# Kernel optimization log

Measured on AMD Instinct MI355X. Metric: run time of the kernel, lower is better.

## Reference

```python
import jax, jax.numpy as jnp
import numpy as np

EMBED_DIM = 256
NUM_CODES = 8192
COMMIT_COST = 0.25


def setup_inputs() -> dict:
    key = jax.random.key(0)
    k1, k2 = jax.random.split(key)
    x = jax.random.normal(k1, (16, 1024, EMBED_DIM), dtype=jnp.float32)
    # torch init is uniform(-1/K, 1/K); use small-scale normal-like init via uniform
    codebook = jax.random.uniform(k2, (NUM_CODES, EMBED_DIM), dtype=jnp.float32,
                                  minval=-1.0 / NUM_CODES, maxval=1.0 / NUM_CODES)
    return {"x": x, "codebook": codebook}


def reference(x, codebook):
    # x: [B, S, D], codebook: [K, D]
    input_shape = x.shape
    flat = x.reshape(-1, EMBED_DIM)  # [N, D]
    distances = (jnp.sum(flat * flat, axis=1, keepdims=True)
                 + jnp.sum(codebook * codebook, axis=1)
                 - 2.0 * jnp.matmul(flat, codebook.T))
    encoding_indices = jnp.argmin(distances, axis=1)  # [N]
    # one-hot @ codebook is just a gather
    quantized = jnp.take(codebook, encoding_indices, axis=0).reshape(input_shape)
    # training w/ EMA: commitment loss only (codebook updated via EMA buffers, not grad)
    commitment_loss = COMMIT_COST * jnp.mean(
        (jax.lax.stop_gradient(quantized) - x) ** 2)
    # straight-through estimator
    quantized_st = x + jax.lax.stop_gradient(quantized - x)
    indices = encoding_indices.reshape(input_shape[:-1])
    return quantized_st, indices, commitment_loss
```

## Files before the change

kernel.cpp:

```cpp
#include <hip/hip_runtime.h>

#define D 256
#define KCODES 8192
#define NTOK 16384
#define QSIZE (NTOK * D)
#define NBLK 128
#define CBS 64
#define TH 2e-4f
#define CBSCALE 4096.0f
#define UNSCALE2 4.8828125e-4f
#define CCAP 4096

typedef _Float16 f16x8 __attribute__((ext_vector_type(8)));
typedef float f32x4 __attribute__((ext_vector_type(4)));
typedef __attribute__((address_space(3))) void* lds_vp;
typedef __attribute__((address_space(1))) const void* gbl_vp;

#define P2_LDS (256 * 65 * 4)

__device__ __forceinline__ ushort f32_to_bf16(float f) {
    unsigned u = __float_as_uint(f);
    return (ushort)((u + 0x7FFFu + ((u >> 16) & 1)) >> 16);
}
__device__ __forceinline__ float bf16_to_f32(ushort h) {
    return __uint_as_float((unsigned)h << 16);
}
__device__ __forceinline__ ushort f32_to_f16(float f) {
    _Float16 h = (_Float16)f;
    ushort u; __builtin_memcpy(&u, &h, 2);
    return u;
}
__device__ __forceinline__ float rdlane(float v, int lane) {
    return __uint_as_float(__builtin_amdgcn_readlane(__float_as_uint(v), lane));
}

__global__ __launch_bounds__(256) void cvtx_kernel(const float* __restrict__ x,
                                                   ushort* __restrict__ xb,
                                                   float* __restrict__ xsq) {
    int i = blockIdx.x * 256 + threadIdx.x;
    float4 v = reinterpret_cast<const float4*>(x)[i];
    ushort4 o;
    o.x = f32_to_f16(v.x); o.y = f32_to_f16(v.y);
    o.z = f32_to_f16(v.z); o.w = f32_to_f16(v.w);
    reinterpret_cast<ushort4*>(xb)[i] = o;
    float s = v.x * v.x + v.y * v.y + v.z * v.z + v.w * v.w;
#pragma unroll
    for (int off = 32; off > 0; off >>= 1) s += __shfl_down(s, off);
    if ((threadIdx.x & 63) == 0) xsq[i >> 6] = s;
}

__global__ __launch_bounds__(256) void e2_kernel(const float* __restrict__ cb,
                                                 float* __restrict__ e2) {
    int c = blockIdx.x * 4 + (threadIdx.x >> 6);
    int lane = threadIdx.x & 63;
    float4 v = reinterpret_cast<const float4*>(cb + (size_t)c * D)[lane];
    float s = v.x * v.x + v.y * v.y + v.z * v.z + v.w * v.w;
#pragma unroll
    for (int off = 32; off > 0; off >>= 1) s += __shfl_down(s, off);
    if (lane == 0) e2[c] = s;
}

__global__ __launch_bounds__(256, 3) void pass1_kernel(
    const ushort* __restrict__ xb, const float* __restrict__ cb,
    const float* __restrict__ e2, unsigned* __restrict__ screen) {
    __shared__ ushort ash[2][128 * 32];
    __shared__ ushort bsh[2][128 * 32];
    const int tid = threadIdx.x;
    const int w = tid >> 6, l = tid & 63;
    const int wr = w >> 1, wc = w & 1;
    const int t0 = blockIdx.x * 128, n0 = blockIdx.y * 128;

    f32x4 acc[4][4];
#pragma unroll
    for (int mt = 0; mt < 4; ++mt)
#pragma unroll
        for (int nt = 0; nt < 4; ++nt) acc[mt][nt] = (f32x4)0.f;

    const int byte0 = w * 2048 + l * 16;
    const int row0 = byte0 >> 6, c80 = (byte0 >> 4) & 3;
    const int byte1 = byte0 + 1024;
    const int row1 = byte1 >> 6, c81 = (byte1 >> 4) & 3;
    const ushort* ga0 = xb + (size_t)(t0 + row0) * D + c80 * 8;
    const ushort* ga1 = xb + (size_t)(t0 + row1) * D + c81 * 8;
    const int brow = tid >> 1, bkh = (tid & 1) * 16;
    const float* gB = cb + (size_t)(n0 + brow) * D + bkh;
    float4 rb[4];

#define STAGE_A(KT, BUF)                                                                   \
    do {                                                                                   \
        __builtin_amdgcn_global_load_lds((gbl_vp)(ga0 + (KT) * 32),                        \
                                         (lds_vp)(&ash[BUF][w * 1024]), 16, 0, 0);         \
        __builtin_amdgcn_global_load_lds((gbl_vp)(ga1 + (KT) * 32),                        \
                                         (lds_vp)(&ash[BUF][w * 1024 + 512]), 16, 0, 0);   \
    } while (0)
#define LOAD_B(KT)                                                                         \
    do {                                                                                   \
        const float4* p = reinterpret_cast<const float4*>(gB + (KT) * 32);                 \
        rb[0] = p[0]; rb[1] = p[1]; rb[2] = p[2]; rb[3] = p[3];                            \
    } while (0)
#define WRITE_B(BUF)                                                                       \
    do {                                                                                   \
        unsigned q[8];                                                                     \
        _Pragma("unroll")                                                                  \
        for (int e = 0; e < 4; ++e) {                                                      \
            q[2 * e] = (unsigned)f32_to_f16(rb[e].x * CBSCALE) |                           \
                       ((unsigned)f32_to_f16(rb[e].y * CBSCALE) << 16);                    \
            q[2 * e + 1] = (unsigned)f32_to_f16(rb[e].z * CBSCALE) |                       \
                           ((unsigned)f32_to_f16(rb[e].w * CBSCALE) << 16);                \
        }                                                                                  \
        uint4* dst = reinterpret_cast<uint4*>(&bsh[BUF][brow * 32 + bkh]);                 \
        uint4 q0; q0.x = q[0]; q0.y = q[1]; q0.z = q[2]; q0.w = q[3];                      \
        uint4 q1; q1.x = q[4]; q1.y = q[5]; q1.z = q[6]; q1.w = q[7];                      \
        dst[0] = q0; dst[1] = q1;                                                          \
    } while (0)

    LOAD_B(0);
    STAGE_A(0, 0);
    WRITE_B(0);
    __syncthreads();
#pragma unroll
    for (int kt = 0; kt < 8; ++kt) {
        const int cur = kt & 1;
        if (kt < 7) { LOAD_B(kt + 1); STAGE_A(kt + 1, cur ^ 1); }
        const ushort* xbase = &ash[cur][0] + (wr * 64 + (l & 15)) * 32 + (l >> 4) * 8;
        const ushort* cbase = &bsh[cur][0] + (wc * 64 + (l & 15)) * 32 + (l >> 4) * 8;
        f16x8 a[4], b[4];
#pragma unroll
        for (int mt = 0; mt < 4; ++mt)
            a[mt] = *reinterpret_cast<const f16x8*>(xbase + mt * 16 * 32);
#pragma unroll
        for (int nt = 0; nt < 4; ++nt)
            b[nt] = *reinterpret_cast<const f16x8*>(cbase + nt * 16 * 32);
#pragma unroll
        for (int mt = 0; mt < 4; ++mt)
#pragma unroll
            for (int nt = 0; nt < 4; ++nt)
                acc[mt][nt] = __builtin_amdgcn_mfma_f32_16x16x32_f16(
                    a[mt], b[nt], acc[mt][nt], 0, 0, 0);
        if (kt < 7) WRITE_B(cur ^ 1);
        __syncthreads();
    }
#undef STAGE_A
#undef LOAD_B
#undef WRITE_B

    float e2v[4];
#pragma unroll
    for (int nt = 0; nt < 4; ++nt)
        e2v[nt] = e2[n0 + wc * 64 + nt * 16 + (l & 15)];
    const int nb64 = blockIdx.y * 2 + wc;
#pragma unroll
    for (int mt = 0; mt < 4; ++mt) {
#pragma unroll
        for (int r = 0; r < 4; ++r) {
            float v1 = fmaf(-UNSCALE2, acc[mt][0][r], e2v[0]);
            float v2 = 3.4e38f;
            int a1 = (l & 15);
#pragma unroll
            for (int nt = 1; nt < 4; ++nt) {
                float f = fmaf(-UNSCALE2, acc[mt][nt][r], e2v[nt]);
                int idx = nt * 16 + (l & 15);
                bool lt = f < v1;
                v2 = lt ? v1 : fminf(v2, f);
                a1 = lt ? idx : a1;
                v1 = lt ? f : v1;
            }
#pragma unroll
            for (int off = 1; off < 16; off <<= 1) {
                float ov1 = __shfl_xor(v1, off);
                float ov2 = __shfl_xor(v2, off);
                int oa1 = __shfl_xor(a1, off);
                float nv2 = fminf(fminf(v2, ov2), fmaxf(v1, ov1));
                bool take = ov1 < v1;
                v1 = take ? ov1 : v1;
                a1 = take ? oa1 : a1;
                v2 = nv2;
            }
            if ((l & 15) == 0) {
                int token = t0 + wr * 64 + mt * 16 + (l >> 4) * 4 + r;
                ushort m1b = f32_to_bf16(v1);
                unsigned big = (v2 - bf16_to_f32(m1b) > TH) ? 1u : 0u;
                screen[(size_t)token * NBLK + nb64] =
                    ((unsigned)m1b << 16) | ((unsigned)a1 << 1) | big;
            }
        }
    }
}

__global__ __launch_bounds__(256) void pass2a_kernel(
    const unsigned* __restrict__ screen, unsigned long long* __restrict__ bestKey,
    unsigned* __restrict__ cand, unsigned* __restrict__ counts,
    float* __restrict__ out) {
    const int tid = threadIdx.x;
    const int w = tid >> 6, l = tid & 63;
    const int token = blockIdx.x * 4 + w;
    if (blockIdx.x == 0 && tid == 0) out[(size_t)QSIZE + NTOK] = 0.f;

    uint2 u2 = reinterpret_cast<const uint2*>(screen + (size_t)token * NBLK)[l];
    float ma = bf16_to_f32((ushort)(u2.x >> 16));
    float mb = bf16_to_f32((ushort)(u2.y >> 16));
    float v1, v2; unsigned pk; int blk;
    if (mb < ma) { v1 = mb; v2 = ma; pk = u2.y; blk = 2 * l + 1; }
    else         { v1 = ma; v2 = mb; pk = u2.x; blk = 2 * l; }
#pragma unroll
    for (int off = 1; off < 64; off <<= 1) {
        float ov1 = __shfl_xor(v1, off);
        float ov2 = __shfl_xor(v2, off);
        unsigned opk = __shfl_xor(pk, off);
        int oblk = __shfl_xor(blk, off);
        float nv2 = fminf(fminf(v2, ov2), fmaxf(v1, ov1));
        bool take = ov1 < v1;
        v1 = take ? ov1 : v1;
        pk = take ? opk : pk;
        blk = take ? oblk : blk;
        v2 = nv2;
    }
    bool decided = ((pk & 1u) != 0u) && (v2 - v1 > TH);
    if (l == 0)
        bestKey[token] = decided
            ? (unsigned long long)(unsigned)(blk * 64 + (int)((pk >> 1) & 63u))
            : 0xFFFFFFFFFFFFFFFFULL;
    if (!decided) {
        float thr = v1 + TH;
        if (ma <= thr) {
            unsigned s = atomicAdd(&counts[2 * l], 1u);
            if (s < CCAP) cand[(size_t)(2 * l) * CCAP + s] = (unsigned)token;
        }
        if (mb <= thr) {
            unsigned s = atomicAdd(&counts[2 * l + 1], 1u);
            if (s < CCAP) cand[(size_t)(2 * l + 1) * CCAP + s] = (unsigned)token;
        }
    }
}

__global__ __launch_bounds__(256, 2) void pass2b_kernel(
    const float* __restrict__ x, const float* __restrict__ cb,
    const float* __restrict__ e2, const float* __restrict__ xsq,
    const unsigned* __restrict__ cand, const unsigned* __restrict__ counts,
    unsigned long long* __restrict__ bestKey) {
    extern __shared__ float csh[];
    const int tid = threadIdx.x;
    const int nb = blockIdx.x >> 2;
    const int quarter = blockIdx.x & 3;
    int cnt = (int)counts[nb];
    if (cnt > CCAP) cnt = CCAP;
    if (quarter * 16 >= cnt) return;

#pragma unroll
    for (int r = 0; r < 16; ++r) {
        int i = r * 256 + tid;
        int row = i >> 6, kq = i & 63;
        float4 v = reinterpret_cast<const float4*>(cb + (size_t)(nb * CBS + row) * D)[kq];
        csh[(kq * 4 + 0) * 65 + row] = v.x;
        csh[(kq * 4 + 1) * 65 + row] = v.y;
        csh[(kq * 4 + 2) * 65 + row] = v.z;
        csh[(kq * 4 + 3) * 65 + row] = v.w;
    }
    __syncthreads();

    const int w = tid >> 6, j = tid & 63;
    const float e2v = e2[nb * CBS + j];
    const int ci0 = nb * CBS + j;
    const float4* X4 = reinterpret_cast<const float4*>(x);
    const unsigned* clist = cand + (size_t)nb * CCAP;
    const int slot = quarter * 4 + w;
    const int p0 = slot * 4;
    if (p0 >= cnt) return;

    for (int p = p0; p < cnt; p += 64) {
        int i1 = p + 1 < cnt ? p + 1 : cnt - 1;
        int i2 = p + 2 < cnt ? p + 2 : cnt - 1;
        int i3 = p + 3 < cnt ? p + 3 : cnt - 1;
        int t0 = (int)clist[p],  t1 = (int)clist[i1];
        int t2 = (int)clist[i2], t3 = (int)clist[i3];
        float4 v0 = X4[(size_t)t0 * 64 + j];
        float4 v1 = X4[(size_t)t1 * 64 + j];
        float4 v2 = X4[(size_t)t2 * 64 + j];
        float4 v3 = X4[(size_t)t3 * 64 + j];
        float a0 = 0.f, a1 = 0.f, a2 = 0.f, a3 = 0.f;
#pragma unroll
        for (int kq = 0; kq < 64; ++kq) {
            float c0 = csh[(kq * 4 + 0) * 65 + j];
            float c1 = csh[(kq * 4 + 1) * 65 + j];
            float c2 = csh[(kq * 4 + 2) * 65 + j];
            float c3 = csh[(kq * 4 + 3) * 65 + j];
            a0 = fmaf(rdlane(v0.x, kq), c0, a0);
            a0 = fmaf(rdlane(v0.y, kq), c1, a0);
            a0 = fmaf(rdlane(v0.z, kq), c2, a0);
            a0 = fmaf(rdlane(v0.w, kq), c3, a0);
            a1 = fmaf(rdlane(v1.x, kq), c0, a1);
            a1 = fmaf(rdlane(v1.y, kq), c1, a1);
            a1 = fmaf(rdlane(v1.z, kq), c2, a1);
            a1 = fmaf(rdlane(v1.w, kq), c3, a1);
            a2 = fmaf(rdlane(v2.x, kq), c0, a2);
            a2 = fmaf(rdlane(v2.y, kq), c1, a2);
            a2 = fmaf(rdlane(v2.z, kq), c2, a2);
            a2 = fmaf(rdlane(v2.w, kq), c3, a2);
            a3 = fmaf(rdlane(v3.x, kq), c0, a3);
            a3 = fmaf(rdlane(v3.y, kq), c1, a3);
            a3 = fmaf(rdlane(v3.z, kq), c2, a3);
            a3 = fmaf(rdlane(v3.w, kq), c3, a3);
        }
        float av[4] = {a0, a1, a2, a3};
        int tv[4] = {t0, t1, t2, t3};
#pragma unroll
        for (int g = 0; g < 4; ++g) {
            float dd = fmaf(-2.f, av[g], xsq[tv[g]] + e2v);
            int ci = ci0;
#pragma unroll
            for (int off = 1; off < 64; off <<= 1) {
                float od = __shfl_xor(dd, off);
                int oc = __shfl_xor(ci, off);
                if (od < dd || (od == dd && oc < ci)) { dd = od; ci = oc; }
            }
            if (j == 0) {
                unsigned u = __float_as_uint(dd);
                u = (u & 0x80000000u) ? ~u : (u | 0x80000000u);
                unsigned long long key =
                    ((unsigned long long)u << 32) | (unsigned)ci;
                atomicMin(bestKey + tv[g], key);
            }
        }
    }
}

__global__ __launch_bounds__(256) void gather_kernel(
    const float* __restrict__ x, const float* __restrict__ cb,
    const unsigned long long* __restrict__ bestKey,
    float* __restrict__ out, float* __restrict__ partial) {
    __shared__ float red[4];
    const int token = blockIdx.x;
    const int tid = threadIdx.x;
    int idx = (int)(bestKey[token] & 0xFFFFFFFFULL);
    if ((unsigned)idx >= (unsigned)KCODES) idx = 0;
    float q = cb[(size_t)idx * D + tid];
    float xv = x[(size_t)token * D + tid];
    out[(size_t)token * D + tid] = q;
    float d = q - xv;
    d = d * d;
#pragma unroll
    for (int off = 32; off > 0; off >>= 1) d += __shfl_down(d, off);
    if ((tid & 63) == 0) red[tid >> 6] = d;
    __syncthreads();
    if (tid == 0) {
        partial[token] = red[0] + red[1] + red[2] + red[3];
        out[(size_t)QSIZE + token] = (float)idx;
    }
}

__global__ __launch_bounds__(256) void loss_kernel(const float* __restrict__ partial,
                                                   float* __restrict__ out) {
    __shared__ float red[4];
    int gid = blockIdx.x * 256 + threadIdx.x;
    float s = partial[gid];
#pragma unroll
    for (int off = 32; off > 0; off >>= 1) s += __shfl_down(s, off);
    if ((threadIdx.x & 63) == 0) red[threadIdx.x >> 6] = s;
    __syncthreads();
    if (threadIdx.x == 0) {
        float total = red[0] + red[1] + red[2] + red[3];
        atomicAdd(out + (size_t)QSIZE + NTOK, 0.25f * total / (float)QSIZE);
    }
}

extern "C" void kernel_launch(void* const* d_in, const int* in_sizes, int n_in,
                              void* d_out, int out_size, void* d_ws, size_t ws_size,
                              hipStream_t stream) {
    const float* x = (const float*)d_in[0];
    const float* cb = (const float*)d_in[1];
    float* out = (float*)d_out;
    float* ws = (float*)d_ws;

    ushort* xb = (ushort*)d_out;
    unsigned* screen = (unsigned*)((char*)d_out + 8388608);
    unsigned* cand = (unsigned*)d_out;

    float* e2 = ws;
    float* xsq = ws + 8192;
    unsigned* counts = (unsigned*)(ws + 8192 + 16384);
    float* partial = ws + 8192 + 2 * 16384;
    unsigned long long* bestKey = (unsigned long long*)(ws + 8192 + 3 * 16384);

    hipFuncSetAttribute((const void*)pass2b_kernel,
                        hipFuncAttributeMaxDynamicSharedMemorySize, P2_LDS);

    cvtx_kernel<<<QSIZE / 1024, 256, 0, stream>>>(x, xb, xsq);
    e2_kernel<<<KCODES / 4, 256, 0, stream>>>(cb, e2);
    pass1_kernel<<<dim3(NTOK / 128, KCODES / 128), 256, 0, stream>>>(xb, cb, e2, screen);
    hipMemsetAsync(counts, 0, NBLK * sizeof(unsigned), stream);
    pass2a_kernel<<<NTOK / 4, 256, 0, stream>>>(screen, bestKey, cand, counts, out);
    pass2b_kernel<<<4 * NBLK, 256, P2_LDS, stream>>>(
        x, cb, e2, xsq, cand, counts, bestKey);
    gather_kernel<<<NTOK, 256, 0, stream>>>(x, cb, bestKey, out, partial);
    loss_kernel<<<NTOK / 256, 256, 0, stream>>>(partial, out);
}
```

Measured before the change: 354.1 us.

## Keep codebook tile resident in LDS and loop over token tiles in pass1

Pass1 now converts a full 128x256 codebook tile to fp16 once per block and keeps it in LDS with an XOR swizzle. Each block then streams 16 token tiles through a double-buffered A stage. Previously every 128x128 output tile reloaded and reconverted its fp32 codebook slice. The aim is to cut repeated global codebook reads and conversion work. In exchange the grid shrinks to 8x64 blocks, occupancy drops to 2 blocks per CU, and the prologue is serialized.

```diff
diff --git a/kernel.cpp b/kernel.cpp
--- a/kernel.cpp
+++ b/kernel.cpp
@@ -16,6 +16,7 @@
 typedef __attribute__((address_space(3))) void* lds_vp;
 typedef __attribute__((address_space(1))) const void* gbl_vp;
 
+#define P1_LDS (128 * 256 * 2 + 2 * 128 * 32 * 2)
 #define P2_LDS (256 * 65 * 4)
 
 __device__ __forceinline__ ushort f32_to_bf16(float f) {
@@ -60,131 +61,135 @@
     if (lane == 0) e2[c] = s;
 }
 
-__global__ __launch_bounds__(256, 3) void pass1_kernel(
+__global__ __launch_bounds__(256, 2) void pass1_kernel(
     const ushort* __restrict__ xb, const float* __restrict__ cb,
     const float* __restrict__ e2, unsigned* __restrict__ screen) {
-    __shared__ ushort ash[2][128 * 32];
-    __shared__ ushort bsh[2][128 * 32];
+    extern __shared__ ushort sm[];
+    ushort* Bsh = sm;
+    ushort* Ash = sm + 128 * 256;
     const int tid = threadIdx.x;
     const int w = tid >> 6, l = tid & 63;
     const int wr = w >> 1, wc = w & 1;
-    const int t0 = blockIdx.x * 128, n0 = blockIdx.y * 128;
-
-    f32x4 acc[4][4];
-#pragma unroll
-    for (int mt = 0; mt < 4; ++mt)
-#pragma unroll
-        for (int nt = 0; nt < 4; ++nt) acc[mt][nt] = (f32x4)0.f;
-
-    const int byte0 = w * 2048 + l * 16;
-    const int row0 = byte0 >> 6, c80 = (byte0 >> 4) & 3;
-    const int byte1 = byte0 + 1024;
-    const int row1 = byte1 >> 6, c81 = (byte1 >> 4) & 3;
-    const ushort* ga0 = xb + (size_t)(t0 + row0) * D + c80 * 8;
-    const ushort* ga1 = xb + (size_t)(t0 + row1) * D + c81 * 8;
-    const int brow = tid >> 1, bkh = (tid & 1) * 16;
-    const float* gB = cb + (size_t)(n0 + brow) * D + bkh;
-    float4 rb[4];
-
-#define STAGE_A(KT, BUF)                                                                   \
+    const int n0 = blockIdx.y * 128;
+    const int tc0 = blockIdx.x * (NTOK / 8);
+
+#pragma unroll
+    for (int j = 0; j < 16; ++j) {
+        int c = tid + j * 256;
+        int row = c >> 5, slot = c & 31;
+        const float4* grow = reinterpret_cast<const float4*>(cb + (size_t)(n0 + row) * D);
+        float4 f0 = grow[slot * 2];
+        float4 f1 = grow[slot * 2 + 1];
+        uint4 q;
+        q.x = (unsigned)f32_to_f16(f0.x * CBSCALE) |
+              ((unsigned)f32_to_f16(f0.y * CBSCALE) << 16);
+        q.y = (unsigned)f32_to_f16(f0.z * CBSCALE) |
+              ((unsigned)f32_to_f16(f0.w * CBSCALE) << 16);
+        q.z = (unsigned)f32_to_f16(f1.x * CBSCALE) |
+              ((unsigned)f32_to_f16(f1.y * CBSCALE) << 16);
+        q.w = (unsigned)f32_to_f16(f1.z * CBSCALE) |
+              ((unsigned)f32_to_f16(f1.w * CBSCALE) << 16);
+        int sw = slot ^ (row & 7);
+        *reinterpret_cast<uint4*>(Bsh + row * 256 + sw * 8) = q;
+    }
+
+    const int arow0 = w * 32 + (l >> 2);
+    const int arow1 = arow0 + 16;
+    const int asg8 = (((l & 3) ^ ((l >> 3) & 3)) << 3);
+
+#define STAGE_A(TB, KT, BUF)                                                               \
     do {                                                                                   \
-        __builtin_amdgcn_global_load_lds((gbl_vp)(ga0 + (KT) * 32),                        \
-                                         (lds_vp)(&ash[BUF][w * 1024]), 16, 0, 0);         \
-        __builtin_amdgcn_global_load_lds((gbl_vp)(ga1 + (KT) * 32),                        \
-                                         (lds_vp)(&ash[BUF][w * 1024 + 512]), 16, 0, 0);   \
+        __builtin_amdgcn_global_load_lds(                                                  \
+            (gbl_vp)(xb + (size_t)((TB) + arow0) * D + (KT) * 32 + asg8),                  \
+            (lds_vp)(Ash + (BUF) * 4096 + w * 1024), 16, 0, 0);                            \
+        __builtin_amdgcn_global_load_lds(                                                  \
+            (gbl_vp)(xb + (size_t)((TB) + arow1) * D + (KT) * 32 + asg8),                  \
+            (lds_vp)(Ash + (BUF) * 4096 + w * 1024 + 512), 16, 0, 0);                      \
     } while (0)
-#define LOAD_B(KT)                                                                         \
-    do {                                                                                   \
-        const float4* p = reinterpret_cast<const float4*>(gB + (KT) * 32);                 \
-        rb[0] = p[0]; rb[1] = p[1]; rb[2] = p[2]; rb[3] = p[3];                            \
-    } while (0)
-#define WRITE_B(BUF)                                                                       \
-    do {                                                                                   \
-        unsigned q[8];                                                                     \
-        _Pragma("unroll")                                                                  \
-        for (int e = 0; e < 4; ++e) {                                                      \
-            q[2 * e] = (unsigned)f32_to_f16(rb[e].x * CBSCALE) |                           \
-                       ((unsigned)f32_to_f16(rb[e].y * CBSCALE) << 16);                    \
-            q[2 * e + 1] = (unsigned)f32_to_f16(rb[e].z * CBSCALE) |                       \
-                           ((unsigned)f32_to_f16(rb[e].w * CBSCALE) << 16);                \
-        }                                                                                  \
-        uint4* dst = reinterpret_cast<uint4*>(&bsh[BUF][brow * 32 + bkh]);                 \
-        uint4 q0; q0.x = q[0]; q0.y = q[1]; q0.z = q[2]; q0.w = q[3];                      \
-        uint4 q1; q1.x = q[4]; q1.y = q[5]; q1.z = q[6]; q1.w = q[7];                      \
-        dst[0] = q0; dst[1] = q1;                                                          \
-    } while (0)
-
-    LOAD_B(0);
-    STAGE_A(0, 0);
-    WRITE_B(0);
-    __syncthreads();
-#pragma unroll
-    for (int kt = 0; kt < 8; ++kt) {
-        const int cur = kt & 1;
-        if (kt < 7) { LOAD_B(kt + 1); STAGE_A(kt + 1, cur ^ 1); }
-        const ushort* xbase = &ash[cur][0] + (wr * 64 + (l & 15)) * 32 + (l >> 4) * 8;
-        const ushort* cbase = &bsh[cur][0] + (wc * 64 + (l & 15)) * 32 + (l >> 4) * 8;
-        f16x8 a[4], b[4];
-#pragma unroll
-        for (int mt = 0; mt < 4; ++mt)
-            a[mt] = *reinterpret_cast<const f16x8*>(xbase + mt * 16 * 32);
-#pragma unroll
-        for (int nt = 0; nt < 4; ++nt)
-            b[nt] = *reinterpret_cast<const f16x8*>(cbase + nt * 16 * 32);
-#pragma unroll
-        for (int mt = 0; mt < 4; ++mt)
-#pragma unroll
-            for (int nt = 0; nt < 4; ++nt)
-                acc[mt][nt] = __builtin_amdgcn_mfma_f32_16x16x32_f16(
-                    a[mt], b[nt], acc[mt][nt], 0, 0, 0);
-        if (kt < 7) WRITE_B(cur ^ 1);
-        __syncthreads();
-    }
-#undef STAGE_A
-#undef LOAD_B
-#undef WRITE_B
+
+    const int qh = l >> 4, l7 = l & 7;
+    const int aslot = qh ^ (((l & 15) >> 1) & 3);
+    const int arow_rd = (wr * 64 + (l & 15)) * 32 + aslot * 8;
+    const int brow_rd = (wc * 64 + (l & 15)) * 256;
 
     float e2v[4];
 #pragma unroll
     for (int nt = 0; nt < 4; ++nt)
         e2v[nt] = e2[n0 + wc * 64 + nt * 16 + (l & 15)];
     const int nb64 = blockIdx.y * 2 + wc;
-#pragma unroll
-    for (int mt = 0; mt < 4; ++mt) {
-#pragma unroll
-        for (int r = 0; r < 4; ++r) {
-            float v1 = fmaf(-UNSCALE2, acc[mt][0][r], e2v[0]);
-            float v2 = 3.4e38f;
-            int a1 = (l & 15);
-#pragma unroll
-            for (int nt = 1; nt < 4; ++nt) {
-                float f = fmaf(-UNSCALE2, acc[mt][nt][r], e2v[nt]);
-                int idx = nt * 16 + (l & 15);
-                bool lt = f < v1;
-                v2 = lt ? v1 : fminf(v2, f);
-                a1 = lt ? idx : a1;
-                v1 = lt ? f : v1;
+
+    STAGE_A(tc0, 0, 0);
+    __syncthreads();
+
+    for (int tt = 0; tt < 16; ++tt) {
+        const int tbase = tc0 + tt * 128;
+        f32x4 acc[4][4];
+#pragma unroll
+        for (int mt = 0; mt < 4; ++mt)
+#pragma unroll
+            for (int nt = 0; nt < 4; ++nt) acc[mt][nt] = (f32x4)0.f;
+#pragma unroll
+        for (int kt = 0; kt < 8; ++kt) {
+            const int cur = kt & 1;
+            if (kt < 7) STAGE_A(tbase, kt + 1, cur ^ 1);
+            else if (tt < 15) STAGE_A(tbase + 128, 0, cur ^ 1);
+            const ushort* abase = Ash + cur * 4096 + arow_rd;
+            f16x8 a[4], b[4];
+#pragma unroll
+            for (int mt = 0; mt < 4; ++mt)
+                a[mt] = *reinterpret_cast<const f16x8*>(abase + mt * 512);
+#pragma unroll
+            for (int nt = 0; nt < 4; ++nt)
+                b[nt] = *reinterpret_cast<const f16x8*>(
+                    Bsh + brow_rd + nt * 4096 + (((kt * 4 + qh) ^ l7) << 3));
+#pragma unroll
+            for (int mt = 0; mt < 4; ++mt)
+#pragma unroll
+                for (int nt = 0; nt < 4; ++nt)
+                    acc[mt][nt] = __builtin_amdgcn_mfma_f32_16x16x32_f16(
+                        a[mt], b[nt], acc[mt][nt], 0, 0, 0);
+            if (kt == 7) {
+#pragma unroll
+                for (int mt = 0; mt < 4; ++mt) {
+#pragma unroll
+                    for (int r = 0; r < 4; ++r) {
+                        float v1 = fmaf(-UNSCALE2, acc[mt][0][r], e2v[0]);
+                        float v2 = 3.4e38f;
+                        int a1 = (l & 15);
+#pragma unroll
+                        for (int nt = 1; nt < 4; ++nt) {
+                            float f = fmaf(-UNSCALE2, acc[mt][nt][r], e2v[nt]);
+                            int idx = nt * 16 + (l & 15);
+                            bool lt = f < v1;
+                            v2 = lt ? v1 : fminf(v2, f);
+                            a1 = lt ? idx : a1;
+                            v1 = lt ? f : v1;
+                        }
+#pragma unroll
+                        for (int off = 1; off < 16; off <<= 1) {
+                            float ov1 = __shfl_xor(v1, off);
+                            float ov2 = __shfl_xor(v2, off);
+                            int oa1 = __shfl_xor(a1, off);
+                            float nv2 = fminf(fminf(v2, ov2), fmaxf(v1, ov1));
+                            bool take = ov1 < v1;
+                            v1 = take ? ov1 : v1;
+                            a1 = take ? oa1 : a1;
+                            v2 = nv2;
+                        }
+                        if ((l & 15) == 0) {
+                            int token = tbase + wr * 64 + mt * 16 + (l >> 4) * 4 + r;
+                            ushort m1b = f32_to_bf16(v1);
+                            unsigned big = (v2 - bf16_to_f32(m1b) > TH) ? 1u : 0u;
+                            screen[(size_t)token * NBLK + nb64] =
+                                ((unsigned)m1b << 16) | ((unsigned)a1 << 1) | big;
+                        }
+                    }
+                }
             }
-#pragma unroll
-            for (int off = 1; off < 16; off <<= 1) {
-                float ov1 = __shfl_xor(v1, off);
-                float ov2 = __shfl_xor(v2, off);
-                int oa1 = __shfl_xor(a1, off);
-                float nv2 = fminf(fminf(v2, ov2), fmaxf(v1, ov1));
-                bool take = ov1 < v1;
-                v1 = take ? ov1 : v1;
-                a1 = take ? oa1 : a1;
-                v2 = nv2;
-            }
-            if ((l & 15) == 0) {
-                int token = t0 + wr * 64 + mt * 16 + (l >> 4) * 4 + r;
-                ushort m1b = f32_to_bf16(v1);
-                unsigned big = (v2 - bf16_to_f32(m1b) > TH) ? 1u : 0u;
-                screen[(size_t)token * NBLK + nb64] =
-                    ((unsigned)m1b << 16) | ((unsigned)a1 << 1) | big;
-            }
+            __syncthreads();
         }
     }
+#undef STAGE_A
 }
 
 __global__ __launch_bounds__(256) void pass2a_kernel(
@@ -381,12 +386,14 @@
     float* partial = ws + 8192 + 2 * 16384;
     unsigned long long* bestKey = (unsigned long long*)(ws + 8192 + 3 * 16384);
 
+    hipFuncSetAttribute((const void*)pass1_kernel,
+                        hipFuncAttributeMaxDynamicSharedMemorySize, P1_LDS);
     hipFuncSetAttribute((const void*)pass2b_kernel,
                         hipFuncAttributeMaxDynamicSharedMemorySize, P2_LDS);
 
     cvtx_kernel<<<QSIZE / 1024, 256, 0, stream>>>(x, xb, xsq);
     e2_kernel<<<KCODES / 4, 256, 0, stream>>>(cb, e2);
-    pass1_kernel<<<dim3(NTOK / 128, KCODES / 128), 256, 0, stream>>>(xb, cb, e2, screen);
+    pass1_kernel<<<dim3(8, KCODES / 128), 256, P1_LDS, stream>>>(xb, cb, e2, screen);
     hipMemsetAsync(counts, 0, NBLK * sizeof(unsigned), stream);
     pass2a_kernel<<<NTOK / 4, 256, 0, stream>>>(screen, bestKey, cand, counts, out);
     pass2b_kernel<<<4 * NBLK, 256, P2_LDS, stream>>>(
```

New measurement: 360.6 us. About the same (+1.9%).
